# Kernel tuning notes

Measured on AMD Instinct MI355X. Metric: run time of the kernel, lower is better.

Reference implementation:

```python
import jax, jax.numpy as jnp
import numpy as np

N = 50000      # nodes per node type
E = 600000     # edges per edge type
H = 128        # hidden_channels (= in_channels)
OUT = 16       # out_channels
G = 64         # number of graphs in the batch
L = 2          # num_layers
NEG_SLOPE = 0.2


def setup_inputs() -> dict:
    key = jax.random.key(0)
    ks = jax.random.split(key, 13)
    x_paper = jax.random.normal(ks[0], (N, H), jnp.float32)
    x_author = jax.random.normal(ks[1], (N, H), jnp.float32)
    edge_pa = jax.random.randint(ks[2], (2, E), 0, N, jnp.int32)   # paper -> author
    edge_ap = jax.random.randint(ks[3], (2, E), 0, N, jnp.int32)   # author -> paper
    batch_paper = jnp.sort(jax.random.randint(ks[4], (N,), 0, G, jnp.int32))
    batch_author = jnp.sort(jax.random.randint(ks[5], (N,), 0, G, jnp.int32))
    # GAT params, stacked [layer, edge_type, ...]; edge_type 0 = paper->author, 1 = author->paper
    Wsrc = jax.random.normal(ks[6], (L, 2, H, H), jnp.float32) * 0.05
    Wdst = jax.random.normal(ks[7], (L, 2, H, H), jnp.float32) * 0.05
    att_src = jax.random.normal(ks[8], (L, 2, H), jnp.float32) * 0.05
    att_dst = jax.random.normal(ks[9], (L, 2, H), jnp.float32) * 0.05
    bias = jax.random.normal(ks[10], (L, 2, H), jnp.float32) * 0.05
    linW = jax.random.normal(ks[11], (H, OUT), jnp.float32) * 0.05
    linb = jax.random.normal(ks[12], (OUT,), jnp.float32) * 0.05
    return {"x_paper": x_paper, "x_author": x_author, "edge_pa": edge_pa,
            "edge_ap": edge_ap, "batch_paper": batch_paper, "batch_author": batch_author,
            "Wsrc": Wsrc, "Wdst": Wdst, "att_src": att_src, "att_dst": att_dst,
            "bias": bias, "linW": linW, "linb": linb}


def _gat(x_s, x_d, edge, Wsrc, Wdst, a_src_w, a_dst_w, b):
    """Single-head PyG GATConv (bipartite, add_self_loops=False, concat)."""
    src, dst = edge[0], edge[1]
    hs = x_s @ Wsrc                        # [Ns, H]
    hd = x_d @ Wdst                        # [Nd, H]
    a_s = hs @ a_src_w                     # [Ns]
    a_d = hd @ a_dst_w                     # [Nd]
    e = jax.nn.leaky_relu(a_s[src] + a_d[dst], NEG_SLOPE)   # [E]
    nd = x_d.shape[0]
    m = jax.ops.segment_max(e, dst, num_segments=nd)        # segment softmax
    ex = jnp.exp(e - m[dst])
    den = jax.ops.segment_sum(ex, dst, num_segments=nd) + 1e-16
    w = ex / den[dst]                                        # [E]
    out = jax.ops.segment_sum(w[:, None] * hs[src], dst, num_segments=nd)
    return out + b


def reference(x_paper, x_author, edge_pa, edge_ap, batch_paper, batch_author,
              Wsrc, Wdst, att_src, att_dst, bias, linW, linb):
    xp, xa = x_paper, x_author
    for l in range(L):
        out_a = _gat(xp, xa, edge_pa, Wsrc[l, 0], Wdst[l, 0], att_src[l, 0], att_dst[l, 0], bias[l, 0])
        out_p = _gat(xa, xp, edge_ap, Wsrc[l, 1], Wdst[l, 1], att_src[l, 1], att_dst[l, 1], bias[l, 1])
        xp = jax.nn.relu(out_p)
        xa = jax.nn.relu(out_a)
    pooled_p = jax.ops.segment_max(xp, batch_paper, num_segments=G)  # [G, H]
    pooled_a = jax.ops.segment_max(xa, batch_author, num_segments=G)
    return (pooled_p @ linW + linb, pooled_a @ linW + linb)
```

## Files before the change

### kernel.cpp

```cpp
#include <hip/hip_runtime.h>
#include <hip/hip_fp16.h>

constexpr int NN = 50000;
constexpr int NE = 600000;
constexpr int HH = 128;
constexpr int GG = 64;
constexpr int LL = 2;
constexpr int OC = 16;
constexpr float NEG = 0.2f;

typedef _Float16 f16x8 __attribute__((ext_vector_type(8)));
typedef float f32x4 __attribute__((ext_vector_type(4)));

__global__ void k_prevec(const float* __restrict__ Wsrc, const float* __restrict__ Wdst,
                         const float* __restrict__ att_src, const float* __restrict__ att_dst,
                         float* __restrict__ v) {
    int b = blockIdx.x;
    int kind = b >> 2, lt = b & 3;
    const float* W   = (kind ? Wdst : Wsrc) + (size_t)lt * HH * HH;
    const float* att = (kind ? att_dst : att_src) + lt * HH;
    __shared__ float sa[HH];
    int t = threadIdx.x;
    sa[t] = att[t];
    __syncthreads();
    float s = 0.f;
    for (int j = 0; j < HH; ++j) s += W[t * HH + j] * sa[j];
    v[b * HH + t] = s;
}

__global__ void k_wcvt(const float* __restrict__ Wsrc, __half* __restrict__ Wt) {
    int lt = blockIdx.x >> 7;
    int nrow = blockIdx.x & 127;
    int k = threadIdx.x;
    Wt[((size_t)lt * HH + nrow) * HH + k] =
        __float2half_rn(Wsrc[(size_t)lt * HH * HH + (size_t)k * HH + nrow]);
}

__global__ void k_hist2(const int* __restrict__ dpa, const int* __restrict__ dap,
                        int* __restrict__ cnt) {
    int i = blockIdx.x * 256 + threadIdx.x;
    if (i < NE) atomicAdd(&cnt[dpa[i]], 1);
    else if (i < 2 * NE) atomicAdd(&cnt[NN + dap[i - NE]], 1);
}

__global__ void k_scan1(const int* __restrict__ cnt, int* __restrict__ bsum, int n) {
    __shared__ int s[256];
    int i = blockIdx.x * 256 + threadIdx.x;
    s[threadIdx.x] = (i < n) ? cnt[i] : 0;
    __syncthreads();
    for (int off = 128; off > 0; off >>= 1) {
        if (threadIdx.x < off) s[threadIdx.x] += s[threadIdx.x + off];
        __syncthreads();
    }
    if (threadIdx.x == 0) bsum[blockIdx.x] = s[0];
}

__global__ void k_scan2(int* __restrict__ bsum, int nb) {
    __shared__ int s[512];
    int t = threadIdx.x;
    int v = (t < nb) ? bsum[t] : 0;
    s[t] = v;
    __syncthreads();
    for (int off = 1; off < 512; off <<= 1) {
        int x = (t >= off) ? s[t - off] : 0;
        __syncthreads();
        s[t] += x;
        __syncthreads();
    }
    if (t < nb) bsum[t] = s[t] - v;
}

__global__ void k_scan3(const int* __restrict__ cnt, const int* __restrict__ bsum,
                        int* __restrict__ rowptr, int n, int e) {
    __shared__ int s[256];
    int t = threadIdx.x;
    int i = blockIdx.x * 256 + t;
    int v = (i < n) ? cnt[i] : 0;
    s[t] = v;
    __syncthreads();
    for (int off = 1; off < 256; off <<= 1) {
        int x = (t >= off) ? s[t - off] : 0;
        __syncthreads();
        s[t] += x;
        __syncthreads();
    }
    if (i < n) rowptr[i] = bsum[blockIdx.x] + s[t] - v;
    if (i == n - 1) rowptr[n] = e;
}

__global__ void k_scatter2(const int* __restrict__ edge_pa, const int* __restrict__ edge_ap,
                           int* __restrict__ cursor, int* __restrict__ col) {
    int i = blockIdx.x * 256 + threadIdx.x;
    if (i < NE) {
        int d = edge_pa[NE + i];
        int p = atomicAdd(&cursor[d], 1);
        col[p] = edge_pa[i];
    } else if (i < 2 * NE) {
        int j = i - NE;
        int d = edge_ap[NE + j];
        int p = atomicAdd(&cursor[NN + d], 1);
        col[p] = edge_ap[j];
    }
}

__global__ __launch_bounds__(256) void k_gemm(const float* __restrict__ X, const __half* __restrict__ Wt,
                                              const float* __restrict__ v1, const float* __restrict__ v2,
                                              __half* __restrict__ Hout,
                                              float* __restrict__ o1, float* __restrict__ o2, int n) {
    int wave = threadIdx.x >> 6;
    int lane = threadIdx.x & 63;
    int r0 = blockIdx.x * 64 + wave * 16;
    int arow = r0 + (lane & 15);
    int kgrp = (lane >> 4) * 8;

    f32x4 acc[8] = {};
    float s1 = 0.f, s2 = 0.f;
#pragma unroll
    for (int ks = 0; ks < 4; ++ks) {
        int k0 = ks * 32 + kgrp;
        float xv[8];
        if (arow < n) {
            float4 x0 = *(const float4*)(X + (size_t)arow * HH + k0);
            float4 x1 = *(const float4*)(X + (size_t)arow * HH + k0 + 4);
            xv[0] = x0.x; xv[1] = x0.y; xv[2] = x0.z; xv[3] = x0.w;
            xv[4] = x1.x; xv[5] = x1.y; xv[6] = x1.z; xv[7] = x1.w;
        } else {
#pragma unroll
            for (int i = 0; i < 8; ++i) xv[i] = 0.f;
        }
        float4 va0 = *(const float4*)(v1 + k0), va1 = *(const float4*)(v1 + k0 + 4);
        float4 vb0 = *(const float4*)(v2 + k0), vb1 = *(const float4*)(v2 + k0 + 4);
        s1 += xv[0] * va0.x + xv[1] * va0.y + xv[2] * va0.z + xv[3] * va0.w
            + xv[4] * va1.x + xv[5] * va1.y + xv[6] * va1.z + xv[7] * va1.w;
        s2 += xv[0] * vb0.x + xv[1] * vb0.y + xv[2] * vb0.z + xv[3] * vb0.w
            + xv[4] * vb1.x + xv[5] * vb1.y + xv[6] * vb1.z + xv[7] * vb1.w;

        f16x8 ahi, alo;
#pragma unroll
        for (int i = 0; i < 8; ++i) {
            _Float16 h = (_Float16)xv[i];
            ahi[i] = h;
            alo[i] = (_Float16)(xv[i] - (float)h);
        }
#pragma unroll
        for (int nt = 0; nt < 8; ++nt) {
            const f16x8 b = *(const f16x8*)(Wt + ((size_t)(nt * 16 + (lane & 15))) * HH + k0);
            acc[nt] = __builtin_amdgcn_mfma_f32_16x16x32_f16(alo, b, acc[nt], 0, 0, 0);
            acc[nt] = __builtin_amdgcn_mfma_f32_16x16x32_f16(ahi, b, acc[nt], 0, 0, 0);
        }
    }

    s1 += __shfl_xor(s1, 16); s1 += __shfl_xor(s1, 32);
    s2 += __shfl_xor(s2, 16); s2 += __shfl_xor(s2, 32);
    if ((lane >> 4) == 0 && arow < n) { o1[arow] = s1; o2[arow] = s2; }

    int srow = r0 + (lane >> 4) * 4;
    int scol = lane & 15;
#pragma unroll
    for (int nt = 0; nt < 8; ++nt) {
#pragma unroll
        for (int reg = 0; reg < 4; ++reg) {
            int gr = srow + reg;
            if (gr < n) Hout[(size_t)gr * HH + nt * 16 + scol] = __float2half_rn(acc[nt][reg]);
        }
    }
}

__global__ __launch_bounds__(256) void k_aggregate2(const int* __restrict__ rpc, const int* __restrict__ colc,
                                                    const __half* __restrict__ H0, const __half* __restrict__ H1,
                                                    const float* __restrict__ as0, const float* __restrict__ ad0,
                                                    const float* __restrict__ as1, const float* __restrict__ ad1,
                                                    const float* __restrict__ bias0, const float* __restrict__ bias1,
                                                    float* __restrict__ XA, float* __restrict__ XP) {
    int w = (blockIdx.x * blockDim.x + threadIdx.x) >> 6;
    int lane = threadIdx.x & 63;
    int type = (w >= NN);
    int node = type ? w - NN : w;
    const int* rowptr = rpc + (type ? NN : 0);
    const __half2* H2  = (const __half2*)(type ? H1 : H0);
    const float* a_s  = type ? as1 : as0;
    float add         = (type ? ad1 : ad0)[node];
    const float* bias = type ? bias1 : bias0;
    float* Xout       = type ? XP : XA;

    int base = rowptr[node], end = rowptr[node + 1];

    float den = 0.f;
    float2 acc = {0.f, 0.f};

    int j = base;
    for (; j + 4 <= end; j += 4) {
        int s0 = colc[j + 0], s1 = colc[j + 1], s2 = colc[j + 2], s3 = colc[j + 3];
        float c0 = a_s[s0] + add, c1 = a_s[s1] + add, c2 = a_s[s2] + add, c3 = a_s[s3] + add;
        __half2 h0 = H2[(size_t)s0 * (HH / 2) + lane];
        __half2 h1 = H2[(size_t)s1 * (HH / 2) + lane];
        __half2 h2 = H2[(size_t)s2 * (HH / 2) + lane];
        __half2 h3 = H2[(size_t)s3 * (HH / 2) + lane];
        c0 = c0 > 0.f ? c0 : NEG * c0;
        c1 = c1 > 0.f ? c1 : NEG * c1;
        c2 = c2 > 0.f ? c2 : NEG * c2;
        c3 = c3 > 0.f ? c3 : NEG * c3;
        float e0 = __expf(c0), e1 = __expf(c1), e2 = __expf(c2), e3 = __expf(c3);
        den += (e0 + e1) + (e2 + e3);
        float2 f0 = __half22float2(h0), f1 = __half22float2(h1);
        float2 f2 = __half22float2(h2), f3 = __half22float2(h3);
        acc.x += e0 * f0.x + e1 * f1.x + e2 * f2.x + e3 * f3.x;
        acc.y += e0 * f0.y + e1 * f1.y + e2 * f2.y + e3 * f3.y;
    }
    for (; j < end; ++j) {
        int s = colc[j];
        float c = a_s[s] + add;
        c = c > 0.f ? c : NEG * c;
        float e = __expf(c);
        den += e;
        float2 f = __half22float2(H2[(size_t)s * (HH / 2) + lane]);
        acc.x += e * f.x;
        acc.y += e * f.y;
    }

    float inv = 1.f / (den + 1e-16f);
    float2 b = *(const float2*)(bias + lane * 2);
    float2 o;
    o.x = fmaxf(acc.x * inv + b.x, 0.f);
    o.y = fmaxf(acc.y * inv + b.y, 0.f);
    *(float2*)(Xout + (size_t)node * HH + lane * 2) = o;
}

constexpr int POOL_CHUNK = 64;
__global__ __launch_bounds__(256) void k_pool(const float* __restrict__ XPf, const float* __restrict__ XAf,
                                              const int* __restrict__ batch_p, const int* __restrict__ batch_a,
                                              unsigned* __restrict__ pooled, int n, int blocksPerType) {
    int type = blockIdx.x / blocksPerType;
    int blk  = blockIdx.x % blocksPerType;
    const float* X = type ? XAf : XPf;
    const int* batch = type ? batch_a : batch_p;
    unsigned* pool = pooled + type * GG * HH;

    int sub  = threadIdx.x >> 5;
    int lane = threadIdx.x & 31;
    int i0 = blk * POOL_CHUNK + sub * (POOL_CHUNK / 8);
    if (i0 >= n) return;
    int i1 = min(i0 + POOL_CHUNK / 8, n);

    int g = batch[i0];
    float4 m = make_float4(0.f, 0.f, 0.f, 0.f);
    for (int i = i0; i < i1; ++i) {
        int gi = batch[i];
        if (gi != g) {
            unsigned* p = pool + g * HH + lane * 4;
            atomicMax(p + 0, __float_as_uint(m.x));
            atomicMax(p + 1, __float_as_uint(m.y));
            atomicMax(p + 2, __float_as_uint(m.z));
            atomicMax(p + 3, __float_as_uint(m.w));
            m = make_float4(0.f, 0.f, 0.f, 0.f);
            g = gi;
        }
        float4 x = *(const float4*)(X + (size_t)i * HH + lane * 4);
        m.x = fmaxf(m.x, x.x);
        m.y = fmaxf(m.y, x.y);
        m.z = fmaxf(m.z, x.z);
        m.w = fmaxf(m.w, x.w);
    }
    unsigned* p = pool + g * HH + lane * 4;
    atomicMax(p + 0, __float_as_uint(m.x));
    atomicMax(p + 1, __float_as_uint(m.y));
    atomicMax(p + 2, __float_as_uint(m.z));
    atomicMax(p + 3, __float_as_uint(m.w));
}

__global__ void k_final(const unsigned* __restrict__ pooled, const float* __restrict__ linW,
                        const float* __restrict__ linb, float* __restrict__ out) {
    int idx = blockIdx.x * blockDim.x + threadIdx.x;
    if (idx >= 2 * GG * OC) return;
    int p = idx >> 10;
    int g = (idx >> 4) & 63;
    int o = idx & 15;
    const unsigned* row = pooled + (size_t)(p * GG + g) * HH;
    float s = linb[o];
    for (int k = 0; k < HH; ++k) s += __uint_as_float(row[k]) * linW[k * OC + o];
    out[idx] = s;
}

extern "C" void kernel_launch(void* const* d_in, const int* in_sizes, int n_in,
                              void* d_out, int out_size, void* d_ws, size_t ws_size,
                              hipStream_t stream) {
    const float* x_paper  = (const float*)d_in[0];
    const float* x_author = (const float*)d_in[1];
    const int*   edge_pa  = (const int*)d_in[2];
    const int*   edge_ap  = (const int*)d_in[3];
    const int*   batch_p  = (const int*)d_in[4];
    const int*   batch_a  = (const int*)d_in[5];
    const float* Wsrc     = (const float*)d_in[6];
    const float* Wdst     = (const float*)d_in[7];
    const float* att_src  = (const float*)d_in[8];
    const float* att_dst  = (const float*)d_in[9];
    const float* bias     = (const float*)d_in[10];
    const float* linW     = (const float*)d_in[11];
    const float* linb     = (const float*)d_in[12];
    float* out = (float*)d_out;

    size_t off = 0;
    char* base = (char*)d_ws;
    auto alloc = [&](size_t bytes) -> void* {
        void* p = base + off;
        off += (bytes + 255) & ~(size_t)255;
        return p;
    };
    __half* H0 = (__half*)alloc((size_t)NN * HH * 2);
    __half* H1 = (__half*)alloc((size_t)NN * HH * 2);
    float* XP  = (float*)alloc((size_t)NN * HH * 4);
    float* XA  = (float*)alloc((size_t)NN * HH * 4);
    float* as0 = (float*)alloc(NN * 4);
    float* ad0 = (float*)alloc(NN * 4);
    float* as1 = (float*)alloc(NN * 4);
    float* ad1 = (float*)alloc(NN * 4);
    float* vv  = (float*)alloc(8 * HH * 4);
    __half* Wt = (__half*)alloc(4 * HH * HH * 2);
    int* rpc  = (int*)alloc((2 * NN + 1) * 4);
    int* colc = (int*)alloc(2 * NE * 4);
    int* cnt  = (int*)alloc(2 * NN * 4);
    int* bsum = (int*)alloc(2048);
    unsigned* pooled = (unsigned*)alloc(2 * GG * HH * 4);

    const int EB2  = (2 * NE + 255) / 256;
    const int NBS2 = (2 * NN + 255) / 256;

    k_prevec<<<8, 128, 0, stream>>>(Wsrc, Wdst, att_src, att_dst, vv);
    k_wcvt<<<512, 128, 0, stream>>>(Wsrc, Wt);

    hipMemsetAsync(cnt, 0, 2 * NN * sizeof(int), stream);
    k_hist2<<<EB2, 256, 0, stream>>>(edge_pa + NE, edge_ap + NE, cnt);
    k_scan1<<<NBS2, 256, 0, stream>>>(cnt, bsum, 2 * NN);
    k_scan2<<<1, 512, 0, stream>>>(bsum, NBS2);
    k_scan3<<<NBS2, 256, 0, stream>>>(cnt, bsum, rpc, 2 * NN, 2 * NE);
    hipMemcpyAsync(cnt, rpc, 2 * NN * sizeof(int), hipMemcpyDeviceToDevice, stream);
    k_scatter2<<<EB2, 256, 0, stream>>>(edge_pa, edge_ap, cnt, colc);

    const float* xp = x_paper;
    const float* xa = x_author;
    const int GB = (NN + 63) / 64;
    for (int l = 0; l < LL; ++l) {
        int t0 = l * 2 + 0, t1 = l * 2 + 1;
        k_gemm<<<GB, 256, 0, stream>>>(xp, Wt + (size_t)t0 * HH * HH,
                                       vv + t0 * HH, vv + (4 + t1) * HH, H0, as0, ad1, NN);
        k_gemm<<<GB, 256, 0, stream>>>(xa, Wt + (size_t)t1 * HH * HH,
                                       vv + t1 * HH, vv + (4 + t0) * HH, H1, as1, ad0, NN);
        k_aggregate2<<<25000, 256, 0, stream>>>(rpc, colc, H0, H1, as0, ad0, as1, ad1,
                                                bias + t0 * HH, bias + t1 * HH, XA, XP);
        xp = XP; xa = XA;
    }

    hipMemsetAsync(pooled, 0, 2 * GG * HH * sizeof(unsigned), stream);
    const int PB = (NN + POOL_CHUNK - 1) / POOL_CHUNK;
    k_pool<<<PB * 2, 256, 0, stream>>>(XP, XA, batch_p, batch_a, pooled, NN, PB);
    k_final<<<8, 256, 0, stream>>>(pooled, linW, linb, out);
}
```

Before: 524.4 us.

## Build CSR via two-pass bucketed scatter and unroll aggregation by eight

Replaces the per-edge global-atomic CSR scatter with a two-level bucket sort. Edges are first binned into 256-node buckets using shared-memory counts and one global atomic per bucket per block. Each bucket is then scattered locally with shared-memory atomics, giving better write locality and less global atomic contention. The aggregation loop also gains an 8-wide unrolled path to put more gathers in flight, at the cost of an extra temp buffer, one more pass over the edges and more registers.

```diff
diff --git a/kernel.cpp b/kernel.cpp
--- a/kernel.cpp
+++ b/kernel.cpp
@@ -8,6 +8,7 @@
 constexpr int LL = 2;
 constexpr int OC = 16;
 constexpr float NEG = 0.2f;
+constexpr int NBK = (2 * NN + 255) / 256;
 
 typedef _Float16 f16x8 __attribute__((ext_vector_type(8)));
 typedef float f32x4 __attribute__((ext_vector_type(4)));
@@ -88,18 +89,54 @@
     if (i == n - 1) rowptr[n] = e;
 }
 
-__global__ void k_scatter2(const int* __restrict__ edge_pa, const int* __restrict__ edge_ap,
-                           int* __restrict__ cursor, int* __restrict__ col) {
-    int i = blockIdx.x * 256 + threadIdx.x;
-    if (i < NE) {
-        int d = edge_pa[NE + i];
-        int p = atomicAdd(&cursor[d], 1);
-        col[p] = edge_pa[i];
-    } else if (i < 2 * NE) {
-        int j = i - NE;
-        int d = edge_ap[NE + j];
-        int p = atomicAdd(&cursor[NN + d], 1);
-        col[p] = edge_ap[j];
+__global__ void k_binit(const int* __restrict__ rpc, int* __restrict__ bcur) {
+    int b = blockIdx.x * 256 + threadIdx.x;
+    if (b < NBK) bcur[b] = rpc[b * 256];
+}
+
+__global__ __launch_bounds__(256) void k_bucket1(const int* __restrict__ edge_pa,
+                                                 const int* __restrict__ edge_ap,
+                                                 int* __restrict__ bcur, unsigned* __restrict__ colt) {
+    __shared__ int cnt[NBK];
+    __shared__ int gpos[NBK];
+    int t = threadIdx.x;
+    int e0 = blockIdx.x * 4096;
+    int m = min(4096, 2 * NE - e0);
+    for (int i = t; i < NBK; i += 256) cnt[i] = 0;
+    __syncthreads();
+    for (int i = t; i < m; i += 256) {
+        int e = e0 + i;
+        int d = (e < NE) ? edge_pa[NE + e] : NN + edge_ap[NE + (e - NE)];
+        atomicAdd(&cnt[d >> 8], 1);
+    }
+    __syncthreads();
+    for (int b = t; b < NBK; b += 256)
+        if (cnt[b]) gpos[b] = atomicAdd(&bcur[b], cnt[b]);
+    __syncthreads();
+    for (int i = t; i < m; i += 256) {
+        int e = e0 + i;
+        int src, d;
+        if (e < NE) { src = edge_pa[e]; d = edge_pa[NE + e]; }
+        else        { int j = e - NE; src = edge_ap[j]; d = NN + edge_ap[NE + j]; }
+        int p = atomicAdd(&gpos[d >> 8], 1);
+        colt[p] = ((unsigned)src << 8) | (unsigned)(d & 255);
+    }
+}
+
+__global__ __launch_bounds__(256) void k_bucket2(const unsigned* __restrict__ colt,
+                                                 const int* __restrict__ rpc, int* __restrict__ colc) {
+    __shared__ int cur[257];
+    int b = blockIdx.x, t = threadIdx.x;
+    int node0 = b * 256;
+    int nn2 = min(256, 2 * NN - node0);
+    for (int i = t; i <= nn2; i += 256) cur[i] = rpc[node0 + i];
+    __syncthreads();
+    int g0 = cur[0], g1 = cur[nn2];
+    __syncthreads();
+    for (int i = g0 + t; i < g1; i += 256) {
+        unsigned p = colt[i];
+        int pos = atomicAdd(&cur[p & 255], 1);
+        colc[pos] = (int)(p >> 8);
     }
 }
 
@@ -176,42 +213,61 @@
     int lane = threadIdx.x & 63;
     int type = (w >= NN);
     int node = type ? w - NN : w;
-    const int* rowptr = rpc + (type ? NN : 0);
     const __half2* H2  = (const __half2*)(type ? H1 : H0);
     const float* a_s  = type ? as1 : as0;
     float add         = (type ? ad1 : ad0)[node];
     const float* bias = type ? bias1 : bias0;
     float* Xout       = type ? XP : XA;
 
-    int base = rowptr[node], end = rowptr[node + 1];
+    int base = rpc[w], end = rpc[w + 1];
 
     float den = 0.f;
     float2 acc = {0.f, 0.f};
 
     int j = base;
+    for (; j + 8 <= end; j += 8) {
+        int s[8]; float c[8]; __half2 h[8];
+#pragma unroll
+        for (int k = 0; k < 8; ++k) s[k] = colc[j + k];
+#pragma unroll
+        for (int k = 0; k < 8; ++k) c[k] = a_s[s[k]] + add;
+#pragma unroll
+        for (int k = 0; k < 8; ++k) h[k] = H2[(size_t)s[k] * (HH / 2) + lane];
+#pragma unroll
+        for (int k = 0; k < 8; ++k) {
+            float cc = c[k];
+            cc = cc > 0.f ? cc : NEG * cc;
+            float e = __expf(cc);
+            den += e;
+            float2 f = __half22float2(h[k]);
+            acc.x += e * f.x;
+            acc.y += e * f.y;
+        }
+    }
     for (; j + 4 <= end; j += 4) {
-        int s0 = colc[j + 0], s1 = colc[j + 1], s2 = colc[j + 2], s3 = colc[j + 3];
-        float c0 = a_s[s0] + add, c1 = a_s[s1] + add, c2 = a_s[s2] + add, c3 = a_s[s3] + add;
-        __half2 h0 = H2[(size_t)s0 * (HH / 2) + lane];
-        __half2 h1 = H2[(size_t)s1 * (HH / 2) + lane];
-        __half2 h2 = H2[(size_t)s2 * (HH / 2) + lane];
-        __half2 h3 = H2[(size_t)s3 * (HH / 2) + lane];
-        c0 = c0 > 0.f ? c0 : NEG * c0;
-        c1 = c1 > 0.f ? c1 : NEG * c1;
-        c2 = c2 > 0.f ? c2 : NEG * c2;
-        c3 = c3 > 0.f ? c3 : NEG * c3;
-        float e0 = __expf(c0), e1 = __expf(c1), e2 = __expf(c2), e3 = __expf(c3);
-        den += (e0 + e1) + (e2 + e3);
-        float2 f0 = __half22float2(h0), f1 = __half22float2(h1);
-        float2 f2 = __half22float2(h2), f3 = __half22float2(h3);
-        acc.x += e0 * f0.x + e1 * f1.x + e2 * f2.x + e3 * f3.x;
-        acc.y += e0 * f0.y + e1 * f1.y + e2 * f2.y + e3 * f3.y;
+        int s[4]; float c[4]; __half2 h[4];
+#pragma unroll
+        for (int k = 0; k < 4; ++k) s[k] = colc[j + k];
+#pragma unroll
+        for (int k = 0; k < 4; ++k) c[k] = a_s[s[k]] + add;
+#pragma unroll
+        for (int k = 0; k < 4; ++k) h[k] = H2[(size_t)s[k] * (HH / 2) + lane];
+#pragma unroll
+        for (int k = 0; k < 4; ++k) {
+            float cc = c[k];
+            cc = cc > 0.f ? cc : NEG * cc;
+            float e = __expf(cc);
+            den += e;
+            float2 f = __half22float2(h[k]);
+            acc.x += e * f.x;
+            acc.y += e * f.y;
+        }
     }
     for (; j < end; ++j) {
         int s = colc[j];
-        float c = a_s[s] + add;
-        c = c > 0.f ? c : NEG * c;
-        float e = __expf(c);
+        float cc = a_s[s] + add;
+        cc = cc > 0.f ? cc : NEG * cc;
+        float e = __expf(cc);
         den += e;
         float2 f = __half22float2(H2[(size_t)s * (HH / 2) + lane]);
         acc.x += e * f.x;
@@ -318,12 +374,15 @@
     __half* Wt = (__half*)alloc(4 * HH * HH * 2);
     int* rpc  = (int*)alloc((2 * NN + 1) * 4);
     int* colc = (int*)alloc(2 * NE * 4);
+    unsigned* colt = (unsigned*)alloc(2 * NE * 4);
     int* cnt  = (int*)alloc(2 * NN * 4);
     int* bsum = (int*)alloc(2048);
+    int* bcur = (int*)alloc(NBK * 4);
     unsigned* pooled = (unsigned*)alloc(2 * GG * HH * 4);
 
     const int EB2  = (2 * NE + 255) / 256;
     const int NBS2 = (2 * NN + 255) / 256;
+    const int CB   = (2 * NE + 4095) / 4096;
 
     k_prevec<<<8, 128, 0, stream>>>(Wsrc, Wdst, att_src, att_dst, vv);
     k_wcvt<<<512, 128, 0, stream>>>(Wsrc, Wt);
@@ -333,8 +392,9 @@
     k_scan1<<<NBS2, 256, 0, stream>>>(cnt, bsum, 2 * NN);
     k_scan2<<<1, 512, 0, stream>>>(bsum, NBS2);
     k_scan3<<<NBS2, 256, 0, stream>>>(cnt, bsum, rpc, 2 * NN, 2 * NE);
-    hipMemcpyAsync(cnt, rpc, 2 * NN * sizeof(int), hipMemcpyDeviceToDevice, stream);
-    k_scatter2<<<EB2, 256, 0, stream>>>(edge_pa, edge_ap, cnt, colc);
+    k_binit<<<(NBK + 255) / 256, 256, 0, stream>>>(rpc, bcur);
+    k_bucket1<<<CB, 256, 0, stream>>>(edge_pa, edge_ap, bcur, colt);
+    k_bucket2<<<NBK, 256, 0, stream>>>(colt, rpc, colc);
 
     const float* xp = x_paper;
     const float* xa = x_author;
```

Result: faster. 450.8 us (-14.0%).
